# Kernel tuning notes

Measured on AMD Instinct MI355X. Metric: run time of the kernel, lower is better.

Reference implementation:

```python
import jax, jax.numpy as jnp
import numpy as np

NB, C, S = 3, 20, 7          # num_boxes, num_classes, gridsize
D = 5 * NB + C               # per-cell channel count = 35
B = 8192


def setup_inputs() -> dict:
    key = jax.random.key(0)
    k1, k2, k3 = jax.random.split(key, 3)
    output = jax.random.uniform(k1, (B, S, S, D), dtype=jnp.float32) * 0.9 + 0.05
    target = jax.random.uniform(k2, (B, S, S, D), dtype=jnp.float32) * 0.9 + 0.05
    # conf channel must be exactly 0 or 1 (obj_mask: conf==1, noobj_mask: conf==0)
    conf = (jax.random.uniform(k3, (B, S, S)) < 0.15).astype(jnp.float32)
    conf_idx = 5 * jnp.arange(NB) + 4          # indices 4, 9, 14
    target = target.at[..., conf_idx].set(conf[..., None])
    return {"output": output, "target": target}


def _to_xyxy(b):
    # b[..., :4] = (cx, cy, w, h); cx,cy are grid-relative (divided by gridsize)
    xy = b[..., :2] / S
    half = 0.5 * b[..., 2:4]
    return jnp.concatenate([xy - half, xy + half], axis=-1)


def reference(output, target):
    nB = output.shape[0]
    out = output.reshape(-1, D)                  # [N, D], N = B*S*S
    tgt = target.reshape(-1, D)
    pbox = out[:, :5 * NB].reshape(-1, NB, 5)    # [N, NB, 5]
    tbox = tgt[:, :5 * NB].reshape(-1, NB, 5)
    pcls = out[:, 5 * NB:]                       # [N, C]
    tcls = tgt[:, 5 * NB:]
    conf_t = tgt[:, 4]
    obj = (conf_t == 1.0).astype(out.dtype)      # [N]
    noobj = (conf_t == 0.0).astype(out.dtype)

    # IoU of each predicted box vs the (single) target box of its cell
    p_xyxy = _to_xyxy(pbox)                      # [N, NB, 4]
    t_xyxy = _to_xyxy(tbox[:, 0, :])[:, None, :] # [N, 1, 4]
    lt = jnp.maximum(p_xyxy[..., :2], t_xyxy[..., :2])
    rb = jnp.minimum(p_xyxy[..., 2:], t_xyxy[..., 2:])
    wh = jnp.clip(rb - lt, 0.0)
    inter = wh[..., 0] * wh[..., 1]              # [N, NB]
    a1 = (p_xyxy[..., 2] - p_xyxy[..., 0]) * (p_xyxy[..., 3] - p_xyxy[..., 1])
    a2 = (t_xyxy[..., 2] - t_xyxy[..., 0]) * (t_xyxy[..., 3] - t_xyxy[..., 1])
    iou = inter / (a1 + a2 - inter)
    best = jnp.argmax(iou, axis=1)               # responsible box index per cell
    max_iou = jnp.max(iou, axis=1)               # [N]
    resp = jax.nn.one_hot(best, NB, dtype=out.dtype) * obj[:, None]  # [N, NB]

    xy_loss = jnp.sum(resp * jnp.sum((pbox[..., :2] - tbox[..., :2]) ** 2, -1))
    wh_loss = jnp.sum(resp * jnp.sum((jnp.sqrt(pbox[..., 2:4]) - jnp.sqrt(tbox[..., 2:4])) ** 2, -1))
    contain_loss = jnp.sum(resp * (pbox[..., 4] - max_iou[:, None]) ** 2)
    class_loss = jnp.sum(obj[:, None] * (pcls - tcls) ** 2)
    noobj_conf_loss = jnp.sum(noobj[:, None] * (pbox[..., 4] - tbox[..., 4]) ** 2)

    coord_scale, noobject_scale = 5.0, 0.5
    return (coord_scale * (xy_loss + wh_loss) + contain_loss
            + noobject_scale * noobj_conf_loss + class_loss) / nB
```

## Files before the change

kernel.cpp:

```cpp
#include <hip/hip_runtime.h>


#define NBOX 3
#define NCLS 20
#define SDIM 7
#define DCH  35
#define CPB  128
#define NTHREADS 128
#define NF4  (CPB * DCH / 4)
#define NF4T (2 * NF4)

typedef __attribute__((address_space(3))) unsigned int  lds_u32;
typedef const __attribute__((address_space(1))) unsigned int glob_u32;

__global__ __launch_bounds__(NTHREADS) void detloss_kernel(
    const float* __restrict__ out_g, const float* __restrict__ tgt_g,
    float* __restrict__ partials, int n_cells, float inv_nB)
{
    __shared__ float4 s_buf[NF4T];
    __shared__ float  s_part[NTHREADS / 64];

    const int tid = threadIdx.x;
    const long long blk_f4 = (long long)blockIdx.x * NF4;
    const float4* go = (const float4*)out_g + blk_f4;
    const float4* gt = (const float4*)tgt_g + blk_f4;

    #pragma unroll
    for (int j = 0; j < 17; ++j) {
        const int k = j * NTHREADS + tid;
        const float4* src = (k < NF4) ? (go + k) : (gt + (k - NF4));
        __builtin_amdgcn_global_load_lds((glob_u32*)src, (lds_u32*)&s_buf[k], 16, 0, 0);
    }
    if (tid < 64) {
        const int k = 17 * NTHREADS + tid;
        __builtin_amdgcn_global_load_lds((glob_u32*)(gt + (k - NF4)),
                                         (lds_u32*)&s_buf[k], 16, 0, 0);
    }
    __syncthreads();

    const float* sf = (const float*)s_buf;
    const float* o = sf + tid * DCH;
    const float* g = sf + 4 * NF4 + tid * DCH;

    const float tx  = g[0] / 7.0f, ty = g[1] / 7.0f;
    const float thw = 0.5f * g[2], thh = 0.5f * g[3];
    const float tx1 = tx - thw, ty1 = ty - thh;
    const float tx2 = tx + thw, ty2 = ty + thh;
    const float a2  = (tx2 - tx1) * (ty2 - ty1);

    const float conf_t = g[4];
    const float obj    = (conf_t == 1.0f) ? 1.0f : 0.0f;
    const float noobj  = (conf_t == 0.0f) ? 1.0f : 0.0f;

    int   best = 0;
    float biou = -__builtin_inff();
    float conf_sq = 0.0f;

    #pragma unroll
    for (int i = 0; i < NBOX; ++i) {
        const float px  = o[5*i]   / 7.0f;
        const float py  = o[5*i+1] / 7.0f;
        const float phw = 0.5f * o[5*i+2];
        const float phh = 0.5f * o[5*i+3];
        const float px1 = px - phw, py1 = py - phh;
        const float px2 = px + phw, py2 = py + phh;

        const float ltx = fmaxf(px1, tx1), lty = fmaxf(py1, ty1);
        const float rbx = fminf(px2, tx2), rby = fminf(py2, ty2);
        const float w = fmaxf(rbx - ltx, 0.0f);
        const float h = fmaxf(rby - lty, 0.0f);
        const float inter = w * h;
        const float a1 = (px2 - px1) * (py2 - py1);
        const float iou = inter / (a1 + a2 - inter);
        if (iou > biou) { biou = iou; best = i; }

        const float dc = o[5*i+4] - g[5*i+4];
        conf_sq += dc * dc;
    }

    float loss = 0.5f * noobj * conf_sq;

    const int b5 = 5 * best;
    const float dx = o[b5]   - g[b5];
    const float dy = o[b5+1] - g[b5+1];
    const float xyl = dx*dx + dy*dy;
    const float dw = sqrtf(o[b5+2]) - sqrtf(g[b5+2]);
    const float dh = sqrtf(o[b5+3]) - sqrtf(g[b5+3]);
    const float whl = dw*dw + dh*dh;
    const float dcf = o[b5+4] - biou;
    const float contain = dcf * dcf;

    float cls = 0.0f;
    #pragma unroll
    for (int c = 0; c < NCLS; ++c) {
        const float d = o[5*NBOX + c] - g[5*NBOX + c];
        cls += d * d;
    }

    loss += obj * (5.0f * (xyl + whl) + contain + cls);
    loss *= inv_nB;

    #pragma unroll
    for (int off = 32; off > 0; off >>= 1)
        loss += __shfl_down(loss, off);
    if ((tid & 63) == 0) s_part[tid >> 6] = loss;
    __syncthreads();
    if (tid == 0) {
        float tot = s_part[0];
        #pragma unroll
        for (int w = 1; w < NTHREADS / 64; ++w) tot += s_part[w];
        partials[blockIdx.x] = tot;
    }
}

__global__ __launch_bounds__(1024) void reduce_kernel(
    const float* __restrict__ partials, float* __restrict__ out, int n)
{
    __shared__ float s[1024 / 64];
    float v = 0.0f;
    for (int i = threadIdx.x; i < n; i += 1024) v += partials[i];
    #pragma unroll
    for (int off = 32; off > 0; off >>= 1)
        v += __shfl_down(v, off);
    if ((threadIdx.x & 63) == 0) s[threadIdx.x >> 6] = v;
    __syncthreads();
    if (threadIdx.x == 0) {
        float t = 0.0f;
        #pragma unroll
        for (int w = 0; w < 1024 / 64; ++w) t += s[w];
        out[0] = t;
    }
}

extern "C" void kernel_launch(void* const* d_in, const int* in_sizes, int n_in,
                              void* d_out, int out_size, void* d_ws, size_t ws_size,
                              hipStream_t stream) {
    const float* out_p = (const float*)d_in[0];
    const float* tgt_p = (const float*)d_in[1];
    float* res  = (float*)d_out;
    float* part = (float*)d_ws;

    const int n_cells = in_sizes[0] / DCH;
    const int nB = n_cells / (SDIM * SDIM);
    const float inv_nB = 1.0f / (float)nB;

    const int blocks = n_cells / CPB;
    hipLaunchKernelGGL(detloss_kernel, dim3(blocks), dim3(NTHREADS), 0, stream,
                       out_p, tgt_p, part, n_cells, inv_nB);
    hipLaunchKernelGGL(reduce_kernel, dim3(1), dim3(1024), 0, stream,
                       part, res, blocks);
}
```

Baseline: 128.9 us.

## Use persistent single-wave blocks with double-buffered LDS prefetch

Replaces one-shot 128-thread blocks with 1024 persistent 64-lane blocks. Each block loops over 64-cell tiles, issuing async global-to-LDS loads for the next tile while computing the current one, and uses vmcnt waits instead of barriers. The reduction now reads exactly one partial per block. This trades the GPU's block-level latency hiding for explicit in-wave prefetch, with fewer waves in flight, which may cut the bandwidth this memory-bound loss can reach. The hardcoded waitcnt encodings are fragile.

```diff
diff --git a/kernel.cpp b/kernel.cpp
--- a/kernel.cpp
+++ b/kernel.cpp
@@ -5,120 +5,135 @@
 #define NCLS 20
 #define SDIM 7
 #define DCH  35
-#define CPB  128
-#define NTHREADS 128
-#define NF4  (CPB * DCH / 4)
-#define NF4T (2 * NF4)
+#define WTILE 64
+#define OUT_UNITS (WTILE * DCH / 4)
+#define UNITS     (2 * OUT_UNITS)
+
+#define WAITCNT_VM18 0x4F72
+#define WAITCNT_VM0  0x0F70
 
 typedef __attribute__((address_space(3))) unsigned int  lds_u32;
 typedef const __attribute__((address_space(1))) unsigned int glob_u32;
 
-__global__ __launch_bounds__(NTHREADS) void detloss_kernel(
+__global__ __launch_bounds__(64) void detloss_kernel(
     const float* __restrict__ out_g, const float* __restrict__ tgt_g,
-    float* __restrict__ partials, int n_cells, float inv_nB)
+    float* __restrict__ partials, int n_tiles, float inv_nB)
 {
-    __shared__ float4 s_buf[NF4T];
-    __shared__ float  s_part[NTHREADS / 64];
+    __shared__ float4 s_buf[2][UNITS];
 
-    const int tid = threadIdx.x;
-    const long long blk_f4 = (long long)blockIdx.x * NF4;
-    const float4* go = (const float4*)out_g + blk_f4;
-    const float4* gt = (const float4*)tgt_g + blk_f4;
+    const int lane  = threadIdx.x;
+    const int wid   = blockIdx.x;
+    const int nwv   = gridDim.x;
 
-    #pragma unroll
-    for (int j = 0; j < 17; ++j) {
-        const int k = j * NTHREADS + tid;
-        const float4* src = (k < NF4) ? (go + k) : (gt + (k - NF4));
-        __builtin_amdgcn_global_load_lds((glob_u32*)src, (lds_u32*)&s_buf[k], 16, 0, 0);
-    }
-    if (tid < 64) {
-        const int k = 17 * NTHREADS + tid;
-        __builtin_amdgcn_global_load_lds((glob_u32*)(gt + (k - NF4)),
-                                         (lds_u32*)&s_buf[k], 16, 0, 0);
-    }
-    __syncthreads();
+    float lane_sum = 0.0f;
 
-    const float* sf = (const float*)s_buf;
-    const float* o = sf + tid * DCH;
-    const float* g = sf + 4 * NF4 + tid * DCH;
+    auto issue = [&](int tile, int buf) {
+        const float4* go = (const float4*)out_g + (long long)tile * OUT_UNITS;
+        const float4* gt = (const float4*)tgt_g + (long long)tile * OUT_UNITS;
+        #pragma unroll
+        for (int j = 0; j < 17; ++j) {
+            const int k = j * 64 + lane;
+            const float4* src = (k < OUT_UNITS) ? (go + k) : (gt + (k - OUT_UNITS));
+            __builtin_amdgcn_global_load_lds((glob_u32*)src, (lds_u32*)&s_buf[buf][k], 16, 0, 0);
+        }
+        if (lane < 32) {
+            const int k = 17 * 64 + lane;
+            __builtin_amdgcn_global_load_lds((glob_u32*)(gt + (k - OUT_UNITS)),
+                                             (lds_u32*)&s_buf[buf][k], 16, 0, 0);
+        }
+    };
 
-    const float tx  = g[0] / 7.0f, ty = g[1] / 7.0f;
-    const float thw = 0.5f * g[2], thh = 0.5f * g[3];
-    const float tx1 = tx - thw, ty1 = ty - thh;
-    const float tx2 = tx + thw, ty2 = ty + thh;
-    const float a2  = (tx2 - tx1) * (ty2 - ty1);
+    auto compute = [&](int buf) {
+        const float* sf = (const float*)&s_buf[buf][0];
+        const float* o  = sf + lane * DCH;
+        const float* g  = sf + 4 * OUT_UNITS + lane * DCH;
 
-    const float conf_t = g[4];
-    const float obj    = (conf_t == 1.0f) ? 1.0f : 0.0f;
-    const float noobj  = (conf_t == 0.0f) ? 1.0f : 0.0f;
+        const float tx  = g[0] / 7.0f, ty = g[1] / 7.0f;
+        const float thw = 0.5f * g[2], thh = 0.5f * g[3];
+        const float tx1 = tx - thw, ty1 = ty - thh;
+        const float tx2 = tx + thw, ty2 = ty + thh;
+        const float a2  = (tx2 - tx1) * (ty2 - ty1);
 
-    int   best = 0;
-    float biou = -__builtin_inff();
-    float conf_sq = 0.0f;
+        const float conf_t = g[4];
+        const float obj    = (conf_t == 1.0f) ? 1.0f : 0.0f;
+        const float noobj  = (conf_t == 0.0f) ? 1.0f : 0.0f;
 
-    #pragma unroll
-    for (int i = 0; i < NBOX; ++i) {
-        const float px  = o[5*i]   / 7.0f;
-        const float py  = o[5*i+1] / 7.0f;
-        const float phw = 0.5f * o[5*i+2];
-        const float phh = 0.5f * o[5*i+3];
-        const float px1 = px - phw, py1 = py - phh;
-        const float px2 = px + phw, py2 = py + phh;
+        int   best = 0;
+        float biou = -__builtin_inff();
+        float conf_sq = 0.0f;
 
-        const float ltx = fmaxf(px1, tx1), lty = fmaxf(py1, ty1);
-        const float rbx = fminf(px2, tx2), rby = fminf(py2, ty2);
-        const float w = fmaxf(rbx - ltx, 0.0f);
-        const float h = fmaxf(rby - lty, 0.0f);
-        const float inter = w * h;
-        const float a1 = (px2 - px1) * (py2 - py1);
-        const float iou = inter / (a1 + a2 - inter);
-        if (iou > biou) { biou = iou; best = i; }
+        #pragma unroll
+        for (int i = 0; i < NBOX; ++i) {
+            const float px  = o[5*i]   / 7.0f;
+            const float py  = o[5*i+1] / 7.0f;
+            const float phw = 0.5f * o[5*i+2];
+            const float phh = 0.5f * o[5*i+3];
+            const float px1 = px - phw, py1 = py - phh;
+            const float px2 = px + phw, py2 = py + phh;
 
-        const float dc = o[5*i+4] - g[5*i+4];
-        conf_sq += dc * dc;
+            const float ltx = fmaxf(px1, tx1), lty = fmaxf(py1, ty1);
+            const float rbx = fminf(px2, tx2), rby = fminf(py2, ty2);
+            const float w = fmaxf(rbx - ltx, 0.0f);
+            const float h = fmaxf(rby - lty, 0.0f);
+            const float inter = w * h;
+            const float a1 = (px2 - px1) * (py2 - py1);
+            const float iou = inter / (a1 + a2 - inter);
+            if (iou > biou) { biou = iou; best = i; }
+
+            const float dc = o[5*i+4] - g[5*i+4];
+            conf_sq += dc * dc;
+        }
+
+        float loss = 0.5f * noobj * conf_sq;
+
+        const int b5 = 5 * best;
+        const float dx = o[b5]   - g[b5];
+        const float dy = o[b5+1] - g[b5+1];
+        const float xyl = dx*dx + dy*dy;
+        const float dw = sqrtf(o[b5+2]) - sqrtf(g[b5+2]);
+        const float dh = sqrtf(o[b5+3]) - sqrtf(g[b5+3]);
+        const float whl = dw*dw + dh*dh;
+        const float dcf = o[b5+4] - biou;
+        const float contain = dcf * dcf;
+
+        float cls = 0.0f;
+        #pragma unroll
+        for (int c = 0; c < NCLS; ++c) {
+            const float d = o[5*NBOX + c] - g[5*NBOX + c];
+            cls += d * d;
+        }
+
+        lane_sum += loss + obj * (5.0f * (xyl + whl) + contain + cls);
+    };
+
+    int cur = wid;
+    if (cur < n_tiles) {
+        issue(cur, 0);
+        int buf = 0;
+        for (int nxt = cur + nwv; nxt < n_tiles; nxt += nwv) {
+            issue(nxt, buf ^ 1);
+            __builtin_amdgcn_s_waitcnt(WAITCNT_VM18);
+            __asm__ __volatile__("" ::: "memory");
+            compute(buf);
+            buf ^= 1;
+        }
+        __builtin_amdgcn_s_waitcnt(WAITCNT_VM0);
+        __asm__ __volatile__("" ::: "memory");
+        compute(buf);
     }
 
-    float loss = 0.5f * noobj * conf_sq;
-
-    const int b5 = 5 * best;
-    const float dx = o[b5]   - g[b5];
-    const float dy = o[b5+1] - g[b5+1];
-    const float xyl = dx*dx + dy*dy;
-    const float dw = sqrtf(o[b5+2]) - sqrtf(g[b5+2]);
-    const float dh = sqrtf(o[b5+3]) - sqrtf(g[b5+3]);
-    const float whl = dw*dw + dh*dh;
-    const float dcf = o[b5+4] - biou;
-    const float contain = dcf * dcf;
-
-    float cls = 0.0f;
-    #pragma unroll
-    for (int c = 0; c < NCLS; ++c) {
-        const float d = o[5*NBOX + c] - g[5*NBOX + c];
-        cls += d * d;
-    }
-
-    loss += obj * (5.0f * (xyl + whl) + contain + cls);
-    loss *= inv_nB;
-
+    float v = lane_sum * inv_nB;
     #pragma unroll
     for (int off = 32; off > 0; off >>= 1)
-        loss += __shfl_down(loss, off);
-    if ((tid & 63) == 0) s_part[tid >> 6] = loss;
-    __syncthreads();
-    if (tid == 0) {
-        float tot = s_part[0];
-        #pragma unroll
-        for (int w = 1; w < NTHREADS / 64; ++w) tot += s_part[w];
-        partials[blockIdx.x] = tot;
-    }
+        v += __shfl_down(v, off);
+    if (lane == 0) partials[wid] = v;
 }
 
 __global__ __launch_bounds__(1024) void reduce_kernel(
     const float* __restrict__ partials, float* __restrict__ out, int n)
 {
     __shared__ float s[1024 / 64];
-    float v = 0.0f;
-    for (int i = threadIdx.x; i < n; i += 1024) v += partials[i];
+    float v = (threadIdx.x < n) ? partials[threadIdx.x] : 0.0f;
     #pragma unroll
     for (int off = 32; off > 0; off >>= 1)
         v += __shfl_down(v, off);
@@ -143,10 +158,11 @@
     const int n_cells = in_sizes[0] / DCH;
     const int nB = n_cells / (SDIM * SDIM);
     const float inv_nB = 1.0f / (float)nB;
+    const int n_tiles = n_cells / WTILE;
 
-    const int blocks = n_cells / CPB;
-    hipLaunchKernelGGL(detloss_kernel, dim3(blocks), dim3(NTHREADS), 0, stream,
-                       out_p, tgt_p, part, n_cells, inv_nB);
+    const int nblocks = 1024;
+    hipLaunchKernelGGL(detloss_kernel, dim3(nblocks), dim3(64), 0, stream,
+                       out_p, tgt_p, part, n_tiles, inv_nB);
     hipLaunchKernelGGL(reduce_kernel, dim3(1), dim3(1024), 0, stream,
-                       part, res, blocks);
+                       part, res, nblocks);
 }
```

Result: no change. 129.7 us (+0.7%).

## Load cells directly into registers instead of staging through LDS

Applied to the files above, without the earlier changes.

Drops the async global-to-LDS staging and barrier. Each thread now loads its own 35-float cell straight into registers with unaligned vector loads, the last load overlapping the previous one. Best-box selection uses selects in place of dynamic indexing, so the arrays can stay in registers, and the block size doubles to 256. The cost is strided, less coalesced per-thread global access (a 140-byte stride) and higher register pressure.

```diff
diff --git a/kernel.cpp b/kernel.cpp
--- a/kernel.cpp
+++ b/kernel.cpp
@@ -5,42 +5,33 @@
 #define NCLS 20
 #define SDIM 7
 #define DCH  35
-#define CPB  128
-#define NTHREADS 128
-#define NF4  (CPB * DCH / 4)
-#define NF4T (2 * NF4)
+#define NTHREADS 256
 
-typedef __attribute__((address_space(3))) unsigned int  lds_u32;
-typedef const __attribute__((address_space(1))) unsigned int glob_u32;
+typedef float float4u __attribute__((ext_vector_type(4), aligned(4)));
 
 __global__ __launch_bounds__(NTHREADS) void detloss_kernel(
     const float* __restrict__ out_g, const float* __restrict__ tgt_g,
-    float* __restrict__ partials, int n_cells, float inv_nB)
+    float* __restrict__ partials, float inv_nB)
 {
-    __shared__ float4 s_buf[NF4T];
-    __shared__ float  s_part[NTHREADS / 64];
+    __shared__ float s_part[NTHREADS / 64];
 
-    const int tid = threadIdx.x;
-    const long long blk_f4 = (long long)blockIdx.x * NF4;
-    const float4* go = (const float4*)out_g + blk_f4;
-    const float4* gt = (const float4*)tgt_g + blk_f4;
+    const int tid  = threadIdx.x;
+    const long long cell = (long long)blockIdx.x * NTHREADS + tid;
+    const float* ob = out_g + cell * DCH;
+    const float* gb = tgt_g + cell * DCH;
 
+    float o[36], g[36];
     #pragma unroll
-    for (int j = 0; j < 17; ++j) {
-        const int k = j * NTHREADS + tid;
-        const float4* src = (k < NF4) ? (go + k) : (gt + (k - NF4));
-        __builtin_amdgcn_global_load_lds((glob_u32*)src, (lds_u32*)&s_buf[k], 16, 0, 0);
+    for (int k = 0; k < 8; ++k) {
+        *(float4u*)&o[4 * k] = *(const float4u*)(ob + 4 * k);
+        *(float4u*)&g[4 * k] = *(const float4u*)(gb + 4 * k);
     }
-    if (tid < 64) {
-        const int k = 17 * NTHREADS + tid;
-        __builtin_amdgcn_global_load_lds((glob_u32*)(gt + (k - NF4)),
-                                         (lds_u32*)&s_buf[k], 16, 0, 0);
+    {
+        float4u to = *(const float4u*)(ob + 31);
+        float4u tg = *(const float4u*)(gb + 31);
+        o[31] = to.x; o[32] = to.y; o[33] = to.z; o[34] = to.w;
+        g[31] = tg.x; g[32] = tg.y; g[33] = tg.z; g[34] = tg.w;
     }
-    __syncthreads();
-
-    const float* sf = (const float*)s_buf;
-    const float* o = sf + tid * DCH;
-    const float* g = sf + 4 * NF4 + tid * DCH;
 
     const float tx  = g[0] / 7.0f, ty = g[1] / 7.0f;
     const float thw = 0.5f * g[2], thh = 0.5f * g[3];
@@ -52,9 +43,10 @@
     const float obj    = (conf_t == 1.0f) ? 1.0f : 0.0f;
     const float noobj  = (conf_t == 0.0f) ? 1.0f : 0.0f;
 
-    int   best = 0;
     float biou = -__builtin_inff();
     float conf_sq = 0.0f;
+    float bo0 = 0.f, bo1 = 0.f, bo2 = 0.f, bo3 = 0.f, bo4 = 0.f;
+    float bg0 = 0.f, bg1 = 0.f, bg2 = 0.f, bg3 = 0.f;
 
     #pragma unroll
     for (int i = 0; i < NBOX; ++i) {
@@ -72,7 +64,18 @@
         const float inter = w * h;
         const float a1 = (px2 - px1) * (py2 - py1);
         const float iou = inter / (a1 + a2 - inter);
-        if (iou > biou) { biou = iou; best = i; }
+
+        const bool better = iou > biou;
+        biou = better ? iou      : biou;
+        bo0  = better ? o[5*i]   : bo0;
+        bo1  = better ? o[5*i+1] : bo1;
+        bo2  = better ? o[5*i+2] : bo2;
+        bo3  = better ? o[5*i+3] : bo3;
+        bo4  = better ? o[5*i+4] : bo4;
+        bg0  = better ? g[5*i]   : bg0;
+        bg1  = better ? g[5*i+1] : bg1;
+        bg2  = better ? g[5*i+2] : bg2;
+        bg3  = better ? g[5*i+3] : bg3;
 
         const float dc = o[5*i+4] - g[5*i+4];
         conf_sq += dc * dc;
@@ -80,14 +83,13 @@
 
     float loss = 0.5f * noobj * conf_sq;
 
-    const int b5 = 5 * best;
-    const float dx = o[b5]   - g[b5];
-    const float dy = o[b5+1] - g[b5+1];
+    const float dx = bo0 - bg0;
+    const float dy = bo1 - bg1;
     const float xyl = dx*dx + dy*dy;
-    const float dw = sqrtf(o[b5+2]) - sqrtf(g[b5+2]);
-    const float dh = sqrtf(o[b5+3]) - sqrtf(g[b5+3]);
+    const float dw = sqrtf(bo2) - sqrtf(bg2);
+    const float dh = sqrtf(bo3) - sqrtf(bg3);
     const float whl = dw*dw + dh*dh;
-    const float dcf = o[b5+4] - biou;
+    const float dcf = bo4 - biou;
     const float contain = dcf * dcf;
 
     float cls = 0.0f;
@@ -144,9 +146,9 @@
     const int nB = n_cells / (SDIM * SDIM);
     const float inv_nB = 1.0f / (float)nB;
 
-    const int blocks = n_cells / CPB;
+    const int blocks = n_cells / NTHREADS;
     hipLaunchKernelGGL(detloss_kernel, dim3(blocks), dim3(NTHREADS), 0, stream,
-                       out_p, tgt_p, part, n_cells, inv_nB);
+                       out_p, tgt_p, part, inv_nB);
     hipLaunchKernelGGL(reduce_kernel, dim3(1), dim3(1024), 0, stream,
                        part, res, blocks);
 }
```

Measured after the change: 148.3 us. +15.1%, slower.
